# Performance work log

Measured on AMD Instinct MI355X. Metric: run time of the kernel, lower is better.

The kernel has to match this reference:

```python
import jax, jax.numpy as jnp
import numpy as np

N = 50000      # nodes
E = 800000     # edges
DIN = 128
DH = 128
DE = 128
DOUT = 2
EPS = 1e-5     # GraphNorm eps


def _xavier(key, fan_in, fan_out):
    lim = float(np.sqrt(6.0 / (fan_in + fan_out)))
    return jax.random.uniform(key, (fan_in, fan_out), jnp.float32, -lim, lim)


def setup_inputs() -> dict:
    key = jax.random.key(0)
    ks = jax.random.split(key, 8)
    x = jax.random.normal(ks[0], (N, DIN), jnp.float32)
    edge_index = jax.random.randint(ks[1], (2, E), 0, N, dtype=jnp.int32)
    W1 = _xavier(ks[2], DIN, DH); b1 = jnp.zeros((DH,), jnp.float32)
    W2 = _xavier(ks[3], DH, DH);  b2 = jnp.zeros((DH,), jnp.float32)
    W3 = _xavier(ks[4], DH, DE);  b3 = jnp.zeros((DE,), jnp.float32)
    gn1_w = jnp.ones((DH,), jnp.float32); gn1_b = jnp.zeros((DH,), jnp.float32); gn1_a = jnp.ones((DH,), jnp.float32)
    gn2_w = jnp.ones((DH,), jnp.float32); gn2_b = jnp.zeros((DH,), jnp.float32); gn2_a = jnp.ones((DH,), jnp.float32)
    Wout = _xavier(ks[5], DE, DOUT); bout = jnp.zeros((DOUT,), jnp.float32)
    return {
        "x": x, "edge_index": edge_index,
        "W1": W1, "b1": b1, "W2": W2, "b2": b2, "W3": W3, "b3": b3,
        "gn1_w": gn1_w, "gn1_b": gn1_b, "gn1_a": gn1_a,
        "gn2_w": gn2_w, "gn2_b": gn2_b, "gn2_a": gn2_a,
        "Wout": Wout, "bout": bout,
    }


def gcn_conv(x, src, dst, W, b):
    # PyG GCNConv: add self-loops, symmetric normalization, linear, scatter-add at dst.
    n = x.shape[0]
    h = x @ W                                   # [N, C]
    loop = jnp.arange(n, dtype=src.dtype)
    s = jnp.concatenate([src, loop])            # [E+N]
    d = jnp.concatenate([dst, loop])
    deg = jnp.zeros((n,), h.dtype).at[d].add(1.0)
    dinv = jnp.where(deg > 0, jax.lax.rsqrt(deg), 0.0)
    norm = dinv[s] * dinv[d]                    # [E+N]
    out = jnp.zeros_like(h).at[d].add(h[s] * norm[:, None])
    return out + b


def graph_norm(h, w, b, alpha):
    # Single-graph GraphNorm: shift by alpha*mean, normalize by variance of shifted values.
    mean = h.mean(axis=0)
    c = h - alpha * mean
    var = (c * c).mean(axis=0)
    return c * jax.lax.rsqrt(var + EPS) * w + b


def reference(x, edge_index, W1, b1, W2, b2, W3, b3,
              gn1_w, gn1_b, gn1_a, gn2_w, gn2_b, gn2_a, Wout, bout):
    src, dst = edge_index[0], edge_index[1]
    h = gcn_conv(x, src, dst, W1, b1)
    h = jax.nn.relu(graph_norm(h, gn1_w, gn1_b, gn1_a))   # dropout identity (eval)
    h = gcn_conv(h, src, dst, W2, b2)
    h = jax.nn.relu(graph_norm(h, gn2_w, gn2_b, gn2_a))
    h = gcn_conv(h, src, dst, W3, b3)
    return h @ Wout + bout
```

## Files before the change

kernel.cpp:

```cpp
#include <hip/hip_runtime.h>

#define GN_EPS 1e-5f


#define HIST_C 64
#define SCAN_CHUNK 4096
#define LDK 136

typedef __attribute__((ext_vector_type(8))) short short8;
typedef __attribute__((ext_vector_type(4))) float f32x4;

__device__ __forceinline__ unsigned short f2bf(float f) {
    unsigned u = __float_as_uint(f);
    u += 0x7fffu + ((u >> 16) & 1u);
    return (unsigned short)(u >> 16);
}
__device__ __forceinline__ float bflo(unsigned u) { return __uint_as_float(u << 16); }
__device__ __forceinline__ float bfhi(unsigned u) { return __uint_as_float(u & 0xffff0000u); }

__global__ __launch_bounds__(256) void k_prep_hist(const float* __restrict__ W1,
                                                   const float* __restrict__ W2,
                                                   const float* __restrict__ W3,
                                                   const float* __restrict__ Wo,
                                                   const float* __restrict__ b3,
                                                   const float* __restrict__ bo,
                                                   unsigned short* __restrict__ Wt,
                                                   float* __restrict__ M,
                                                   float* __restrict__ mb,
                                                   const int* __restrict__ dst,
                                                   unsigned short* __restrict__ cnt,
                                                   unsigned short* __restrict__ pos,
                                                   int e, int n, int chunk) {
    __shared__ __align__(16) unsigned bins[32768];
    if (blockIdx.x < 2) {
        unsigned short* sT = (unsigned short*)bins;
        const float* W = blockIdx.x == 0 ? W1 : W2;
        unsigned short* o = Wt + blockIdx.x * 16384;
        const float4* W4 = (const float4*)W;
        for (int idx = threadIdx.x; idx < 128 * 32; idx += 256) {
            int k = idx >> 5, c4 = idx & 31;
            float4 v = W4[k * 32 + c4];
            sT[(c4 * 4 + 0) * 130 + k] = f2bf(v.x);
            sT[(c4 * 4 + 1) * 130 + k] = f2bf(v.y);
            sT[(c4 * 4 + 2) * 130 + k] = f2bf(v.z);
            sT[(c4 * 4 + 3) * 130 + k] = f2bf(v.w);
        }
        __syncthreads();
        for (int idx = threadIdx.x; idx < 128 * 128; idx += 256) {
            int c = idx >> 7, k = idx & 127;
            o[idx] = sT[c * 130 + k];
        }
    } else if (blockIdx.x == 2) {
        int k = threadIdx.x;
        if (k < 128) {
            float m0 = 0.f, m1 = 0.f;
            for (int c = 0; c < 128; ++c) {
                float w = W3[k * 128 + c];
                m0 += w * Wo[c * 2];
                m1 += w * Wo[c * 2 + 1];
            }
            M[k * 2] = m0;
            M[k * 2 + 1] = m1;
            if (k < 2) {
                float s = 0.f;
                for (int c = 0; c < 128; ++c) s += b3[c] * Wo[c * 2 + k];
                mb[k] = s + bo[k];
            }
        }
    } else {
        const int c = (int)blockIdx.x - 3;
        const int c0 = c * chunk;
        const int c1 = (c0 + chunk < e) ? c0 + chunk : e;
        const int nw = (n + 1) >> 1;
        for (int i = threadIdx.x; i < nw; i += 256) bins[i] = 0u;
        __syncthreads();
        const bool al = ((size_t)dst & 15) == 0;
        for (int i = c0 + (int)threadIdx.x * 4; i < c1; i += 1024) {
            if (al && i + 3 < c1) {
                int4 d4 = *(const int4*)(dst + i);
                unsigned o0 = atomicAdd(&bins[(unsigned)d4.x >> 1],
                                        (d4.x & 1) ? 0x10000u : 1u);
                unsigned o1 = atomicAdd(&bins[(unsigned)d4.y >> 1],
                                        (d4.y & 1) ? 0x10000u : 1u);
                unsigned o2 = atomicAdd(&bins[(unsigned)d4.z >> 1],
                                        (d4.z & 1) ? 0x10000u : 1u);
                unsigned o3 = atomicAdd(&bins[(unsigned)d4.w >> 1],
                                        (d4.w & 1) ? 0x10000u : 1u);
                ushort4 p;
                p.x = (unsigned short)((o0 >> ((d4.x & 1) * 16)) & 0xffffu);
                p.y = (unsigned short)((o1 >> ((d4.y & 1) * 16)) & 0xffffu);
                p.z = (unsigned short)((o2 >> ((d4.z & 1) * 16)) & 0xffffu);
                p.w = (unsigned short)((o3 >> ((d4.w & 1) * 16)) & 0xffffu);
                *(ushort4*)(pos + i) = p;
            } else {
                for (int k = i; k < c1 && k < i + 4; ++k) {
                    int d = dst[k];
                    unsigned old = atomicAdd(&bins[(unsigned)d >> 1],
                                             (d & 1) ? 0x10000u : 1u);
                    pos[k] = (unsigned short)((old >> ((d & 1) * 16)) & 0xffffu);
                }
            }
        }
        __syncthreads();
        unsigned short* cr = cnt + (size_t)c * n;
        if ((n & 1) == 0) {
            unsigned* cr32 = (unsigned*)cr;
            for (int i = threadIdx.x; i < (n >> 1); i += 256) cr32[i] = bins[i];
        } else {
            for (int i = threadIdx.x; i < n; i += 256)
                cr[i] = (unsigned short)((bins[i >> 1] >> ((i & 1) * 16)) & 0xffffu);
        }
    }
}

__global__ __launch_bounds__(256) void k_reduce(unsigned short* __restrict__ cnt,
                                                int* __restrict__ degi,
                                                int* __restrict__ partial,
                                                int n, int nchunks) {
    int node = blockIdx.x * 256 + threadIdx.x;
    int pdeg = 0;
    if (node < n) {
        int s = 0;
        int cb = 0;
        for (; cb + 8 <= nchunks; cb += 8) {
            int v[8];
            #pragma unroll
            for (int q = 0; q < 8; ++q) v[q] = cnt[(size_t)(cb + q) * n + node];
            #pragma unroll
            for (int q = 0; q < 8; ++q) {
                cnt[(size_t)(cb + q) * n + node] = (unsigned short)s;
                s += v[q];
            }
        }
        for (; cb < nchunks; ++cb) {
            size_t id = (size_t)cb * n + node;
            int v = cnt[id];
            cnt[id] = (unsigned short)s;
            s += v;
        }
        degi[node] = s;
        pdeg = (s + 7) & ~7;
    }
    #pragma unroll
    for (int off = 32; off; off >>= 1) pdeg += __shfl_down(pdeg, off);
    __shared__ int ws[4];
    if ((threadIdx.x & 63) == 0) ws[threadIdx.x >> 6] = pdeg;
    __syncthreads();
    if (threadIdx.x == 0) partial[blockIdx.x] = ws[0] + ws[1] + ws[2] + ws[3];
}

__global__ __launch_bounds__(256) void k_scanfinal(const int* __restrict__ degi,
                                                   const int* __restrict__ partial,
                                                   int* __restrict__ rowptr,
                                                   float* __restrict__ dinv, int n, int nb) {
    int blockbase = 0;
    for (int i = 0; i < (int)blockIdx.x * 16; ++i) blockbase += partial[i];

    int base = blockIdx.x * SCAN_CHUNK + threadIdx.x * 16;
    int v[16], pv[16];
    int s = 0;
    #pragma unroll
    for (int q = 0; q < 16; ++q) {
        int i = base + q;
        v[q] = (i < n) ? degi[i] : 0;
        pv[q] = (v[q] + 7) & ~7;
        s += pv[q];
    }
    const int lane = threadIdx.x & 63;
    const int wid = threadIdx.x >> 6;
    int x = s;
    #pragma unroll
    for (int off = 1; off < 64; off <<= 1) {
        int t = __shfl_up(x, off);
        if (lane >= off) x += t;
    }
    __shared__ int ws[4];
    if (lane == 63) ws[wid] = x;
    __syncthreads();
    int waveoff = 0;
    if (wid > 0) waveoff += ws[0];
    if (wid > 1) waveoff += ws[1];
    if (wid > 2) waveoff += ws[2];
    int excl = x - s + waveoff + blockbase;
    #pragma unroll
    for (int q = 0; q < 16; ++q) {
        int i = base + q;
        if (i < n) {
            rowptr[i] = excl;
            dinv[i] = rsqrtf((float)(v[q] + 1));
        }
        excl += pv[q];
    }
    if ((int)blockIdx.x == nb - 1 && threadIdx.x == 255) {
        rowptr[n] = excl;
    }
}

__global__ void k_fill(const int* __restrict__ src, const int* __restrict__ dst,
                       const unsigned short* __restrict__ pos,
                       const unsigned short* __restrict__ pref,
                       const int* __restrict__ rowptr,
                       const float* __restrict__ dinv,
                       unsigned* __restrict__ csr_ew, int e, int n, int chunk) {
    int base = (blockIdx.x * blockDim.x + threadIdx.x) * 4;
    if (base >= e) return;
    const unsigned short* pr = pref + (size_t)(base / chunk) * n;
    if (base + 3 < e && (((size_t)src & 15) == 0) && (((size_t)dst & 15) == 0)) {
        int4 s4 = *(const int4*)(src + base);
        int4 d4 = *(const int4*)(dst + base);
        ushort4 p4 = *(const ushort4*)(pos + base);
        float as0 = dinv[s4.x], as1 = dinv[s4.y], as2 = dinv[s4.z], as3 = dinv[s4.w];
        float ad0 = dinv[d4.x], ad1 = dinv[d4.y], ad2 = dinv[d4.z], ad3 = dinv[d4.w];
        int b0 = rowptr[d4.x] + pr[d4.x] + p4.x;
        int b1 = rowptr[d4.y] + pr[d4.y] + p4.y;
        int b2 = rowptr[d4.z] + pr[d4.z] + p4.z;
        int b3 = rowptr[d4.w] + pr[d4.w] + p4.w;
        csr_ew[b0] = ((unsigned)s4.x << 16) | (unsigned)f2bf(as0 * ad0);
        csr_ew[b1] = ((unsigned)s4.y << 16) | (unsigned)f2bf(as1 * ad1);
        csr_ew[b2] = ((unsigned)s4.z << 16) | (unsigned)f2bf(as2 * ad2);
        csr_ew[b3] = ((unsigned)s4.w << 16) | (unsigned)f2bf(as3 * ad3);
    } else {
        for (int i = base; i < e && i < base + 4; ++i) {
            int s = src[i], d = dst[i];
            float w = dinv[s] * dinv[d];
            csr_ew[rowptr[d] + (int)pr[d] + (int)pos[i]] =
                ((unsigned)s << 16) | (unsigned)f2bf(w);
        }
    }
}

__global__ __launch_bounds__(256) void k_gemm_f32(const float* __restrict__ X,
                                                  const unsigned short* __restrict__ Wt,
                                                  unsigned short* __restrict__ Y,
                                                  int nrows) {
    __shared__ __align__(16) unsigned short sB[128 * LDK];
    const int t = threadIdx.x;
    const int row0 = blockIdx.x * 64;

    for (int idx = t; idx < 128 * 16; idx += 256) {
        int c = idx >> 4, ch = idx & 15;
        uint4 v = ((const uint4*)(Wt + c * 128))[ch];
        *(uint4*)(&sB[c * LDK + ch * 8]) = v;
    }

    const int w = t >> 6;
    const int lane = t & 63;
    const int m = lane & 15;
    const int quad = lane >> 4;

    const int grow_a = row0 + w * 16 + m;
    const int srow = grow_a < nrows ? grow_a : 0;
    const float4* Xr = (const float4*)(X + (size_t)srow * 128);
    short8 a[4];
    #pragma unroll
    for (int ks = 0; ks < 4; ++ks) {
        int ko4 = ks * 8 + quad * 2;
        float4 v0 = Xr[ko4];
        float4 v1 = Xr[ko4 + 1];
        short8 av;
        av[0] = (short)f2bf(v0.x); av[1] = (short)f2bf(v0.y);
        av[2] = (short)f2bf(v0.z); av[3] = (short)f2bf(v0.w);
        av[4] = (short)f2bf(v1.x); av[5] = (short)f2bf(v1.y);
        av[6] = (short)f2bf(v1.z); av[7] = (short)f2bf(v1.w);
        a[ks] = av;
    }
    __syncthreads();

    f32x4 acc[8] = {};
    #pragma unroll
    for (int ks = 0; ks < 4; ++ks) {
        int ko = ks * 32 + quad * 8;
        #pragma unroll
        for (int ct = 0; ct < 8; ++ct) {
            short8 b = *(const short8*)(&sB[(ct * 16 + m) * LDK + ko]);
            acc[ct] = __builtin_amdgcn_mfma_f32_16x16x32_bf16(a[ks], b, acc[ct], 0, 0, 0);
        }
    }
    #pragma unroll
    for (int r = 0; r < 4; ++r) {
        int grow = row0 + w * 16 + quad * 4 + r;
        if (grow >= nrows) continue;
        unsigned short* yr = Y + (size_t)grow * 128 + m;
        #pragma unroll
        for (int ct = 0; ct < 8; ++ct) yr[ct * 16] = f2bf(acc[ct][r]);
    }
}

__global__ __launch_bounds__(256) void k_gemm_bf(const unsigned short* __restrict__ Xb,
                                                 const unsigned short* __restrict__ Wt,
                                                 unsigned short* __restrict__ Y,
                                                 const float* __restrict__ cs,
                                                 const float* __restrict__ cb,
                                                 int nrows) {
    __shared__ __align__(16) unsigned short sB[128 * LDK];
    const int t = threadIdx.x;
    const int row0 = blockIdx.x * 64;

    for (int idx = t; idx < 128 * 16; idx += 256) {
        int c = idx >> 4, ch = idx & 15;
        uint4 v = ((const uint4*)(Wt + c * 128))[ch];
        *(uint4*)(&sB[c * LDK + ch * 8]) = v;
    }

    const int w = t >> 6;
    const int lane = t & 63;
    const int m = lane & 15;
    const int quad = lane >> 4;

    const int grow_a = row0 + w * 16 + m;
    const int srow = grow_a < nrows ? grow_a : 0;
    const uint4* Xr = (const uint4*)(Xb + (size_t)srow * 128);
    short8 a[4];
    #pragma unroll
    for (int ks = 0; ks < 4; ++ks) {
        uint4 u = Xr[ks * 4 + quad];
        int kf = (ks * 32 + quad * 8) >> 2;
        float4 s0 = ((const float4*)cs)[kf];
        float4 s1 = ((const float4*)cs)[kf + 1];
        float4 c0 = ((const float4*)cb)[kf];
        float4 c1 = ((const float4*)cb)[kf + 1];
        short8 av;
        av[0] = (short)f2bf(fmaxf(fmaf(bflo(u.x), s0.x, c0.x), 0.f));
        av[1] = (short)f2bf(fmaxf(fmaf(bfhi(u.x), s0.y, c0.y), 0.f));
        av[2] = (short)f2bf(fmaxf(fmaf(bflo(u.y), s0.z, c0.z), 0.f));
        av[3] = (short)f2bf(fmaxf(fmaf(bfhi(u.y), s0.w, c0.w), 0.f));
        av[4] = (short)f2bf(fmaxf(fmaf(bflo(u.z), s1.x, c1.x), 0.f));
        av[5] = (short)f2bf(fmaxf(fmaf(bfhi(u.z), s1.y, c1.y), 0.f));
        av[6] = (short)f2bf(fmaxf(fmaf(bflo(u.w), s1.z, c1.z), 0.f));
        av[7] = (short)f2bf(fmaxf(fmaf(bfhi(u.w), s1.w, c1.w), 0.f));
        a[ks] = av;
    }
    __syncthreads();

    f32x4 acc[8] = {};
    #pragma unroll
    for (int ks = 0; ks < 4; ++ks) {
        int ko = ks * 32 + quad * 8;
        #pragma unroll
        for (int ct = 0; ct < 8; ++ct) {
            short8 b = *(const short8*)(&sB[(ct * 16 + m) * LDK + ko]);
            acc[ct] = __builtin_amdgcn_mfma_f32_16x16x32_bf16(a[ks], b, acc[ct], 0, 0, 0);
        }
    }
    #pragma unroll
    for (int r = 0; r < 4; ++r) {
        int grow = row0 + w * 16 + quad * 4 + r;
        if (grow >= nrows) continue;
        unsigned short* yr = Y + (size_t)grow * 128 + m;
        #pragma unroll
        for (int ct = 0; ct < 8; ++ct) yr[ct * 16] = f2bf(acc[ct][r]);
    }
}

__global__ __launch_bounds__(256) void k_gather(const unsigned short* __restrict__ H,
                                                unsigned short* __restrict__ O,
                                                const int* __restrict__ rowptr,
                                                const unsigned* __restrict__ csr_ew,
                                                const float* __restrict__ dinv,
                                                const float* __restrict__ bias,
                                                float* __restrict__ pS,
                                                float* __restrict__ pQ, int n) {
    __shared__ float sS[4][128];
    __shared__ float sQ[4][128];
    const int wid = threadIdx.x >> 6;
    const int node = blockIdx.x * 4 + wid;
    const int lane = threadIdx.x & 63;
    const int qw = lane >> 4;
    const int ql = lane & 15;
    const uint4* Hx = (const uint4*)H;
    float acc[8] = {};
    if (node < n) {
        float di = dinv[node];
        if (qw == 0) {
            uint4 u = Hx[(size_t)node * 16 + ql];
            float dd = di * di;
            float4 ba = ((const float4*)bias)[ql * 2];
            float4 bb = ((const float4*)bias)[ql * 2 + 1];
            acc[0] = bflo(u.x) * dd + ba.x; acc[1] = bfhi(u.x) * dd + ba.y;
            acc[2] = bflo(u.y) * dd + ba.z; acc[3] = bfhi(u.y) * dd + ba.w;
            acc[4] = bflo(u.z) * dd + bb.x; acc[5] = bfhi(u.z) * dd + bb.y;
            acc[6] = bflo(u.w) * dd + bb.z; acc[7] = bfhi(u.w) * dd + bb.w;
        }
        int j = rowptr[node];
        const int end = rowptr[node + 1];
        for (; j + 16 <= end; j += 16) {
            unsigned ew[4];
            #pragma unroll
            for (int q = 0; q < 4; ++q) ew[q] = csr_ew[j + 4 * q + qw];
            uint4 u[4];
            #pragma unroll
            for (int q = 0; q < 4; ++q)
                u[q] = Hx[((ew[q] >> 12) & 0xFFFF0u) + (unsigned)ql];
            #pragma unroll
            for (int q = 0; q < 4; ++q) {
                float nr = __uint_as_float(ew[q] << 16);
                acc[0] += bflo(u[q].x) * nr; acc[1] += bfhi(u[q].x) * nr;
                acc[2] += bflo(u[q].y) * nr; acc[3] += bfhi(u[q].y) * nr;
                acc[4] += bflo(u[q].z) * nr; acc[5] += bfhi(u[q].z) * nr;
                acc[6] += bflo(u[q].w) * nr; acc[7] += bfhi(u[q].w) * nr;
            }
        }
        if (j < end) {
            unsigned ew[2];
            #pragma unroll
            for (int q = 0; q < 2; ++q) ew[q] = csr_ew[j + qw * 2 + q];
            uint4 u[2];
            #pragma unroll
            for (int q = 0; q < 2; ++q)
                u[q] = Hx[((ew[q] >> 12) & 0xFFFF0u) + (unsigned)ql];
            #pragma unroll
            for (int q = 0; q < 2; ++q) {
                float nr = __uint_as_float(ew[q] << 16);
                acc[0] += bflo(u[q].x) * nr; acc[1] += bfhi(u[q].x) * nr;
                acc[2] += bflo(u[q].y) * nr; acc[3] += bfhi(u[q].y) * nr;
                acc[4] += bflo(u[q].z) * nr; acc[5] += bfhi(u[q].z) * nr;
                acc[6] += bflo(u[q].w) * nr; acc[7] += bfhi(u[q].w) * nr;
            }
        }
        #pragma unroll
        for (int i = 0; i < 8; ++i) {
            acc[i] += __shfl_down(acc[i], 32);
            acc[i] += __shfl_down(acc[i], 16);
        }
    }
    if (qw == 0) {
        if (node < n) {
            unsigned short h[8];
            float v[8];
            #pragma unroll
            for (int i = 0; i < 8; ++i) {
                h[i] = f2bf(acc[i]);
                v[i] = __uint_as_float((unsigned)h[i] << 16);
                sS[wid][ql * 8 + i] = v[i];
                sQ[wid][ql * 8 + i] = v[i] * v[i];
            }
            uint4 o;
            o.x = (unsigned)h[0] | ((unsigned)h[1] << 16);
            o.y = (unsigned)h[2] | ((unsigned)h[3] << 16);
            o.z = (unsigned)h[4] | ((unsigned)h[5] << 16);
            o.w = (unsigned)h[6] | ((unsigned)h[7] << 16);
            *(uint4*)(O + (size_t)node * 128 + ql * 8) = o;
        } else {
            #pragma unroll
            for (int i = 0; i < 8; ++i) {
                sS[wid][ql * 8 + i] = 0.f;
                sQ[wid][ql * 8 + i] = 0.f;
            }
        }
    }
    __syncthreads();
    const int t = threadIdx.x;
    if (t < 128) {
        float s = sS[0][t] + sS[1][t] + sS[2][t] + sS[3][t];
        float q = sQ[0][t] + sQ[1][t] + sQ[2][t] + sQ[3][t];
        const int slotb = (blockIdx.x & 63) << 7;
        atomicAdd(&pS[slotb + t], s);
        atomicAdd(&pQ[slotb + t], q);
    }
}

__global__ __launch_bounds__(256) void k_zproj(const unsigned short* __restrict__ Xb,
                                               const float* __restrict__ M,
                                               const float* __restrict__ cs,
                                               const float* __restrict__ cb,
                                               float2* __restrict__ Z, int n) {
    int node = blockIdx.x * 4 + (threadIdx.x >> 6);
    if (node >= n) return;
    int lane = threadIdx.x & 63;
    unsigned u = ((const unsigned*)Xb)[(size_t)node * 64 + lane];
    int c0 = lane * 2;
    float a = fmaxf(fmaf(bflo(u), cs[c0], cb[c0]), 0.f);
    float b = fmaxf(fmaf(bfhi(u), cs[c0 + 1], cb[c0 + 1]), 0.f);
    float p0 = a * M[c0 * 2]     + b * M[(c0 + 1) * 2];
    float p1 = a * M[c0 * 2 + 1] + b * M[(c0 + 1) * 2 + 1];
    #pragma unroll
    for (int off = 32; off; off >>= 1) {
        p0 += __shfl_down(p0, off);
        p1 += __shfl_down(p1, off);
    }
    if (lane == 0) Z[node] = make_float2(p0, p1);
}

__global__ __launch_bounds__(256) void k_gatherZ(const float2* __restrict__ Z,
                                                 const int* __restrict__ rowptr,
                                                 const unsigned* __restrict__ csr_ew,
                                                 const float* __restrict__ dinv,
                                                 const float* __restrict__ mb,
                                                 float* __restrict__ out, int n) {
    int wid = threadIdx.x >> 6;
    int lane = threadIdx.x & 63;
    int g = lane >> 4;
    int gl = lane & 15;
    int node = blockIdx.x * 16 + wid * 4 + g;
    if (node >= n) return;
    float2 acc = make_float2(0.f, 0.f);
    if (gl == 0) {
        float di = dinv[node];
        float2 z = Z[node];
        acc.x = z.x * di * di + mb[0];
        acc.y = z.y * di * di + mb[1];
    }
    int j = rowptr[node];
    const int end = rowptr[node + 1];
    for (int jj = j + gl; jj < end; jj += 16) {
        unsigned ew = csr_ew[jj];
        float2 z = Z[ew >> 16];
        float w = __uint_as_float(ew << 16);
        acc.x += z.x * w;
        acc.y += z.y * w;
    }
    #pragma unroll
    for (int off = 8; off; off >>= 1) {
        acc.x += __shfl_down(acc.x, off);
        acc.y += __shfl_down(acc.y, off);
    }
    if (gl == 0) {
        out[(size_t)node * 2]     = acc.x;
        out[(size_t)node * 2 + 1] = acc.y;
    }
}

__global__ void k_finstats(const float* __restrict__ pS, const float* __restrict__ pQ,
                           const float* __restrict__ w, const float* __restrict__ b,
                           const float* __restrict__ alpha,
                           float* __restrict__ colscale, float* __restrict__ colshift,
                           int n) {
    int c = threadIdx.x;
    if (c >= 128) return;
    float s = 0.f, q = 0.f;
    #pragma unroll 8
    for (int blk = 0; blk < 64; ++blk) {
        s += pS[blk * 128 + c];
        q += pQ[blk * 128 + c];
    }
    float inv_n = 1.0f / (float)n;
    float m = s * inv_n;
    float eh2 = q * inv_n;
    float a = alpha[c];
    float var = eh2 - (2.0f * a - a * a) * m * m;
    float scale = rsqrtf(var + GN_EPS) * w[c];
    colscale[c] = scale;
    colshift[c] = b[c] - a * m * scale;
}

extern "C" void kernel_launch(void* const* d_in, const int* in_sizes, int n_in,
                              void* d_out, int out_size, void* d_ws, size_t ws_size,
                              hipStream_t stream) {
    const float* x    = (const float*)d_in[0];
    const int*   ei   = (const int*)  d_in[1];
    const float* W1   = (const float*)d_in[2];
    const float* b1   = (const float*)d_in[3];
    const float* W2   = (const float*)d_in[4];
    const float* b2   = (const float*)d_in[5];
    const float* W3   = (const float*)d_in[6];
    const float* b3   = (const float*)d_in[7];
    const float* gn1w = (const float*)d_in[8];
    const float* gn1b = (const float*)d_in[9];
    const float* gn1a = (const float*)d_in[10];
    const float* gn2w = (const float*)d_in[11];
    const float* gn2b = (const float*)d_in[12];
    const float* gn2a = (const float*)d_in[13];
    const float* Wout = (const float*)d_in[14];
    const float* bout = (const float*)d_in[15];
    float* out = (float*)d_out;

    const int n = in_sizes[0] / 128;
    const int e = in_sizes[1] / 2;
    const int* srcI = ei;
    const int* dstI = ei + e;

    const int chunk = (((e + HIST_C - 1) / HIST_C) + 3) & ~3;
    const int nchunks = (e + chunk - 1) / chunk;

    char* base = (char*)d_ws;
    size_t off = 0;
    auto take = [&](size_t bytes) -> void* {
        void* r = base + off;
        off += (bytes + 15) & ~(size_t)15;
        return r;
    };
    unsigned short* bufH = (unsigned short*)take((size_t)n * 256);
    unsigned short* bufG = (unsigned short*)take((size_t)n * 256);
    float* dinv     = (float*)take((size_t)n * 4);
    float* colscale = (float*)take(128 * 4);
    float* colshift = (float*)take(128 * 4);
    int*   rowptr   = (int*)take(((size_t)n + 1) * 4);
    int*   partial  = (int*)take(256 * 4);
    unsigned short* Wt = (unsigned short*)take(2 * 16384 * 2);
    float* M        = (float*)take(256 * 4);
    float* mb       = (float*)take(2 * 4);
    float2* Z       = (float2*)take((size_t)n * 8);
    int*   degi     = (int*)take((size_t)n * 4);
    unsigned short* cnt = (unsigned short*)take((size_t)nchunks * n * 2);
    unsigned short* pos = (unsigned short*)take((size_t)e * 2);
    float* pS       = (float*)take(2 * 64 * 128 * 4);
    float* pQ       = (float*)take(2 * 64 * 128 * 4);
    size_t csr_cap  = (size_t)e + 8 * (size_t)n;
    unsigned* csr_ew = (unsigned*)take(csr_cap * 4);
    size_t zbytes   = (size_t)((base + off) - (char*)pS);

    const int nb = (n + SCAN_CHUNK - 1) / SCAN_CHUNK;
    const int gemmGrid = (n + 63) / 64;
    const int gathGrid = (n + 3) / 4;

    hipMemsetAsync(pS, 0, zbytes, stream);
    k_prep_hist<<<3 + nchunks, 256, 0, stream>>>(W1, W2, W3, Wout, b3, bout,
                                                 Wt, M, mb, dstI, cnt, pos, e, n, chunk);
    k_reduce<<<(n + 255) / 256, 256, 0, stream>>>(cnt, degi, partial, n, nchunks);
    k_scanfinal<<<nb, 256, 0, stream>>>(degi, partial, rowptr, dinv, n, nb);
    k_fill<<<(e + 1023) / 1024, 256, 0, stream>>>(srcI, dstI, pos, cnt, rowptr,
                                                  dinv, csr_ew, e, n, chunk);

    k_gemm_f32<<<gemmGrid, 256, 0, stream>>>(x, Wt, bufH, n);
    k_gather<<<gathGrid, 256, 0, stream>>>(bufH, bufG, rowptr, csr_ew, dinv, b1, pS, pQ, n);
    k_finstats<<<1, 128, 0, stream>>>(pS, pQ, gn1w, gn1b, gn1a, colscale, colshift, n);

    k_gemm_bf<<<gemmGrid, 256, 0, stream>>>(bufG, Wt + 16384, bufH, colscale, colshift, n);
    k_gather<<<gathGrid, 256, 0, stream>>>(bufH, bufG, rowptr, csr_ew, dinv, b2,
                                           pS + 8192, pQ + 8192, n);
    k_finstats<<<1, 128, 0, stream>>>(pS + 8192, pQ + 8192, gn2w, gn2b, gn2a,
                                      colscale, colshift, n);

    k_zproj<<<gathGrid, 256, 0, stream>>>(bufG, M, colscale, colshift, Z, n);
    k_gatherZ<<<(n + 15) / 16, 256, 0, stream>>>(Z, rowptr, csr_ew, dinv, mb, out, n);
}
```

Baseline: 265.9 us.

## Fuse CSR fill with first GEMM, inline GraphNorm stats, drop memset

```diff
diff --git a/kernel.cpp b/kernel.cpp
--- a/kernel.cpp
+++ b/kernel.cpp
@@ -27,6 +27,8 @@
                                                    unsigned short* __restrict__ Wt,
                                                    float* __restrict__ M,
                                                    float* __restrict__ mb,
+                                                   float* __restrict__ pS,
+                                                   float* __restrict__ pQ,
                                                    const int* __restrict__ dst,
                                                    unsigned short* __restrict__ cnt,
                                                    unsigned short* __restrict__ pos,
@@ -51,6 +53,11 @@
             o[idx] = sT[c * 130 + k];
         }
     } else if (blockIdx.x == 2) {
+        float4 z4 = make_float4(0.f, 0.f, 0.f, 0.f);
+        for (int i = threadIdx.x; i < 4096; i += 256) {
+            ((float4*)pS)[i] = z4;
+            ((float4*)pQ)[i] = z4;
+        }
         int k = threadIdx.x;
         if (k < 128) {
             float m0 = 0.f, m1 = 0.f;
@@ -152,7 +159,9 @@
 __global__ __launch_bounds__(256) void k_scanfinal(const int* __restrict__ degi,
                                                    const int* __restrict__ partial,
                                                    int* __restrict__ rowptr,
-                                                   float* __restrict__ dinv, int n, int nb) {
+                                                   float* __restrict__ dinv,
+                                                   unsigned* __restrict__ csr_ew,
+                                                   int n, int nb) {
     int blockbase = 0;
     for (int i = 0; i < (int)blockIdx.x * 16; ++i) blockbase += partial[i];
 
@@ -188,6 +197,7 @@
         if (i < n) {
             rowptr[i] = excl;
             dinv[i] = rsqrtf((float)(v[q] + 1));
+            for (int z = v[q]; z < pv[q]; ++z) csr_ew[excl + z] = 0u;
         }
         excl += pv[q];
     }
@@ -196,46 +206,63 @@
     }
 }
 
-__global__ void k_fill(const int* __restrict__ src, const int* __restrict__ dst,
-                       const unsigned short* __restrict__ pos,
-                       const unsigned short* __restrict__ pref,
-                       const int* __restrict__ rowptr,
-                       const float* __restrict__ dinv,
-                       unsigned* __restrict__ csr_ew, int e, int n, int chunk) {
-    int base = (blockIdx.x * blockDim.x + threadIdx.x) * 4;
-    if (base >= e) return;
-    const unsigned short* pr = pref + (size_t)(base / chunk) * n;
-    if (base + 3 < e && (((size_t)src & 15) == 0) && (((size_t)dst & 15) == 0)) {
-        int4 s4 = *(const int4*)(src + base);
-        int4 d4 = *(const int4*)(dst + base);
-        ushort4 p4 = *(const ushort4*)(pos + base);
-        float as0 = dinv[s4.x], as1 = dinv[s4.y], as2 = dinv[s4.z], as3 = dinv[s4.w];
-        float ad0 = dinv[d4.x], ad1 = dinv[d4.y], ad2 = dinv[d4.z], ad3 = dinv[d4.w];
-        int b0 = rowptr[d4.x] + pr[d4.x] + p4.x;
-        int b1 = rowptr[d4.y] + pr[d4.y] + p4.y;
-        int b2 = rowptr[d4.z] + pr[d4.z] + p4.z;
-        int b3 = rowptr[d4.w] + pr[d4.w] + p4.w;
-        csr_ew[b0] = ((unsigned)s4.x << 16) | (unsigned)f2bf(as0 * ad0);
-        csr_ew[b1] = ((unsigned)s4.y << 16) | (unsigned)f2bf(as1 * ad1);
-        csr_ew[b2] = ((unsigned)s4.z << 16) | (unsigned)f2bf(as2 * ad2);
-        csr_ew[b3] = ((unsigned)s4.w << 16) | (unsigned)f2bf(as3 * ad3);
-    } else {
-        for (int i = base; i < e && i < base + 4; ++i) {
-            int s = src[i], d = dst[i];
-            float w = dinv[s] * dinv[d];
-            csr_ew[rowptr[d] + (int)pr[d] + (int)pos[i]] =
-                ((unsigned)s << 16) | (unsigned)f2bf(w);
-        }
-    }
-}
-
-__global__ __launch_bounds__(256) void k_gemm_f32(const float* __restrict__ X,
+__global__ __launch_bounds__(256) void k_fillgemm(const float* __restrict__ X,
                                                   const unsigned short* __restrict__ Wt,
                                                   unsigned short* __restrict__ Y,
-                                                  int nrows) {
+                                                  const int* __restrict__ src,
+                                                  const int* __restrict__ dst,
+                                                  const unsigned short* __restrict__ pos,
+                                                  const unsigned short* __restrict__ pref,
+                                                  const int* __restrict__ rowptr,
+                                                  const float* __restrict__ dinv,
+                                                  unsigned* __restrict__ csr_ew,
+                                                  int nrows, int e, int chunk, int n,
+                                                  int ngemm, int nfill) {
     __shared__ __align__(16) unsigned short sB[128 * LDK];
+
+    int mn2 = (ngemm < nfill ? ngemm : nfill) * 2;
+    bool isg;
+    int bid;
+    if ((int)blockIdx.x < mn2) {
+        isg = (blockIdx.x & 1) == 0;
+        bid = blockIdx.x >> 1;
+    } else {
+        int r = (int)blockIdx.x - mn2;
+        isg = ngemm > nfill;
+        bid = (mn2 >> 1) + r;
+    }
+
+    if (!isg) {
+        int base = (bid * 256 + (int)threadIdx.x) * 4;
+        if (base >= e) return;
+        const unsigned short* pr = pref + (size_t)(base / chunk) * n;
+        if (base + 3 < e && (((size_t)src & 15) == 0) && (((size_t)dst & 15) == 0)) {
+            int4 s4 = *(const int4*)(src + base);
+            int4 d4 = *(const int4*)(dst + base);
+            ushort4 p4 = *(const ushort4*)(pos + base);
+            float as0 = dinv[s4.x], as1 = dinv[s4.y], as2 = dinv[s4.z], as3 = dinv[s4.w];
+            float ad0 = dinv[d4.x], ad1 = dinv[d4.y], ad2 = dinv[d4.z], ad3 = dinv[d4.w];
+            int b0 = rowptr[d4.x] + pr[d4.x] + p4.x;
+            int b1 = rowptr[d4.y] + pr[d4.y] + p4.y;
+            int b2 = rowptr[d4.z] + pr[d4.z] + p4.z;
+            int b3 = rowptr[d4.w] + pr[d4.w] + p4.w;
+            csr_ew[b0] = ((unsigned)s4.x << 16) | (unsigned)f2bf(as0 * ad0);
+            csr_ew[b1] = ((unsigned)s4.y << 16) | (unsigned)f2bf(as1 * ad1);
+            csr_ew[b2] = ((unsigned)s4.z << 16) | (unsigned)f2bf(as2 * ad2);
+            csr_ew[b3] = ((unsigned)s4.w << 16) | (unsigned)f2bf(as3 * ad3);
+        } else {
+            for (int i = base; i < e && i < base + 4; ++i) {
+                int s = src[i], d = dst[i];
+                float w = dinv[s] * dinv[d];
+                csr_ew[rowptr[d] + (int)pr[d] + (int)pos[i]] =
+                    ((unsigned)s << 16) | (unsigned)f2bf(w);
+            }
+        }
+        return;
+    }
+
     const int t = threadIdx.x;
-    const int row0 = blockIdx.x * 64;
+    const int row0 = bid * 64;
 
     for (int idx = t; idx < 128 * 16; idx += 256) {
         int c = idx >> 4, ch = idx & 15;
@@ -286,21 +313,54 @@
     }
 }
 
+__device__ __forceinline__ void finstats_lds(const float* __restrict__ pS,
+                                             const float* __restrict__ pQ,
+                                             const float* __restrict__ gw,
+                                             const float* __restrict__ gb,
+                                             const float* __restrict__ ga,
+                                             float* __restrict__ sCS,
+                                             float* __restrict__ sCB, int n) {
+    int c = threadIdx.x;
+    if (c < 128) {
+        float s = 0.f, q = 0.f;
+        #pragma unroll 8
+        for (int blk = 0; blk < 64; ++blk) {
+            s += pS[blk * 128 + c];
+            q += pQ[blk * 128 + c];
+        }
+        float inv_n = 1.0f / (float)n;
+        float m = s * inv_n;
+        float eh2 = q * inv_n;
+        float a = ga[c];
+        float var = eh2 - (2.0f * a - a * a) * m * m;
+        float scale = rsqrtf(var + GN_EPS) * gw[c];
+        sCS[c] = scale;
+        sCB[c] = gb[c] - a * m * scale;
+    }
+}
+
 __global__ __launch_bounds__(256) void k_gemm_bf(const unsigned short* __restrict__ Xb,
                                                  const unsigned short* __restrict__ Wt,
                                                  unsigned short* __restrict__ Y,
-                                                 const float* __restrict__ cs,
-                                                 const float* __restrict__ cb,
-                                                 int nrows) {
+                                                 const float* __restrict__ pS,
+                                                 const float* __restrict__ pQ,
+                                                 const float* __restrict__ gw,
+                                                 const float* __restrict__ gb,
+                                                 const float* __restrict__ ga,
+                                                 int nrows, int n) {
     __shared__ __align__(16) unsigned short sB[128 * LDK];
+    __shared__ __align__(16) float sCS[128];
+    __shared__ __align__(16) float sCB[128];
     const int t = threadIdx.x;
     const int row0 = blockIdx.x * 64;
 
+    finstats_lds(pS, pQ, gw, gb, ga, sCS, sCB, n);
     for (int idx = t; idx < 128 * 16; idx += 256) {
         int c = idx >> 4, ch = idx & 15;
         uint4 v = ((const uint4*)(Wt + c * 128))[ch];
         *(uint4*)(&sB[c * LDK + ch * 8]) = v;
     }
+    __syncthreads();
 
     const int w = t >> 6;
     const int lane = t & 63;
@@ -315,10 +375,10 @@
     for (int ks = 0; ks < 4; ++ks) {
         uint4 u = Xr[ks * 4 + quad];
         int kf = (ks * 32 + quad * 8) >> 2;
-        float4 s0 = ((const float4*)cs)[kf];
-        float4 s1 = ((const float4*)cs)[kf + 1];
-        float4 c0 = ((const float4*)cb)[kf];
-        float4 c1 = ((const float4*)cb)[kf + 1];
+        float4 s0 = ((const float4*)sCS)[kf];
+        float4 s1 = ((const float4*)sCS)[kf + 1];
+        float4 c0 = ((const float4*)sCB)[kf];
+        float4 c1 = ((const float4*)sCB)[kf + 1];
         short8 av;
         av[0] = (short)f2bf(fmaxf(fmaf(bflo(u.x), s0.x, c0.x), 0.f));
         av[1] = (short)f2bf(fmaxf(fmaf(bfhi(u.x), s0.y, c0.y), 0.f));
@@ -330,7 +390,6 @@
         av[7] = (short)f2bf(fmaxf(fmaf(bfhi(u.w), s1.w, c1.w), 0.f));
         a[ks] = av;
     }
-    __syncthreads();
 
     f32x4 acc[8] = {};
     #pragma unroll
@@ -461,24 +520,46 @@
 
 __global__ __launch_bounds__(256) void k_zproj(const unsigned short* __restrict__ Xb,
                                                const float* __restrict__ M,
-                                               const float* __restrict__ cs,
-                                               const float* __restrict__ cb,
+                                               const float* __restrict__ pS,
+                                               const float* __restrict__ pQ,
+                                               const float* __restrict__ gw,
+                                               const float* __restrict__ gb,
+                                               const float* __restrict__ ga,
                                                float2* __restrict__ Z, int n) {
-    int node = blockIdx.x * 4 + (threadIdx.x >> 6);
-    if (node >= n) return;
-    int lane = threadIdx.x & 63;
-    unsigned u = ((const unsigned*)Xb)[(size_t)node * 64 + lane];
-    int c0 = lane * 2;
-    float a = fmaxf(fmaf(bflo(u), cs[c0], cb[c0]), 0.f);
-    float b = fmaxf(fmaf(bfhi(u), cs[c0 + 1], cb[c0 + 1]), 0.f);
-    float p0 = a * M[c0 * 2]     + b * M[(c0 + 1) * 2];
-    float p1 = a * M[c0 * 2 + 1] + b * M[(c0 + 1) * 2 + 1];
-    #pragma unroll
-    for (int off = 32; off; off >>= 1) {
-        p0 += __shfl_down(p0, off);
-        p1 += __shfl_down(p1, off);
-    }
-    if (lane == 0) Z[node] = make_float2(p0, p1);
+    __shared__ __align__(16) float sCS[128];
+    __shared__ __align__(16) float sCB[128];
+    __shared__ __align__(16) float sM[256];
+    finstats_lds(pS, pQ, gw, gb, ga, sCS, sCB, n);
+    if (threadIdx.x < 128) {
+        sM[threadIdx.x * 2] = M[threadIdx.x * 2];
+        sM[threadIdx.x * 2 + 1] = M[threadIdx.x * 2 + 1];
+    }
+    __syncthreads();
+
+    const int wid = threadIdx.x >> 6;
+    const int lane = threadIdx.x & 63;
+    const int c0 = lane * 2;
+    const float cs0 = sCS[c0], cs1 = sCS[c0 + 1];
+    const float cb0 = sCB[c0], cb1 = sCB[c0 + 1];
+    const float m00 = sM[c0 * 2], m01 = sM[c0 * 2 + 1];
+    const float m10 = sM[(c0 + 1) * 2], m11 = sM[(c0 + 1) * 2 + 1];
+
+    #pragma unroll
+    for (int p = 0; p < 16; ++p) {
+        int node = (int)blockIdx.x * 64 + p * 4 + wid;
+        if (node >= n) break;
+        unsigned u = ((const unsigned*)Xb)[(size_t)node * 64 + lane];
+        float a = fmaxf(fmaf(bflo(u), cs0, cb0), 0.f);
+        float b = fmaxf(fmaf(bfhi(u), cs1, cb1), 0.f);
+        float p0 = a * m00 + b * m10;
+        float p1 = a * m01 + b * m11;
+        #pragma unroll
+        for (int off = 32; off; off >>= 1) {
+            p0 += __shfl_down(p0, off);
+            p1 += __shfl_down(p1, off);
+        }
+        if (lane == 0) Z[node] = make_float2(p0, p1);
+    }
 }
 
 __global__ __launch_bounds__(256) void k_gatherZ(const float2* __restrict__ Z,
@@ -518,29 +599,6 @@
         out[(size_t)node * 2]     = acc.x;
         out[(size_t)node * 2 + 1] = acc.y;
     }
-}
-
-__global__ void k_finstats(const float* __restrict__ pS, const float* __restrict__ pQ,
-                           const float* __restrict__ w, const float* __restrict__ b,
-                           const float* __restrict__ alpha,
-                           float* __restrict__ colscale, float* __restrict__ colshift,
-                           int n) {
-    int c = threadIdx.x;
-    if (c >= 128) return;
-    float s = 0.f, q = 0.f;
-    #pragma unroll 8
-    for (int blk = 0; blk < 64; ++blk) {
-        s += pS[blk * 128 + c];
-        q += pQ[blk * 128 + c];
-    }
-    float inv_n = 1.0f / (float)n;
-    float m = s * inv_n;
-    float eh2 = q * inv_n;
-    float a = alpha[c];
-    float var = eh2 - (2.0f * a - a * a) * m * m;
-    float scale = rsqrtf(var + GN_EPS) * w[c];
-    colscale[c] = scale;
-    colshift[c] = b[c] - a * m * scale;
 }
 
 extern "C" void kernel_launch(void* const* d_in, const int* in_sizes, int n_in,
@@ -582,8 +640,6 @@
     unsigned short* bufH = (unsigned short*)take((size_t)n * 256);
     unsigned short* bufG = (unsigned short*)take((size_t)n * 256);
     float* dinv     = (float*)take((size_t)n * 4);
-    float* colscale = (float*)take(128 * 4);
-    float* colshift = (float*)take(128 * 4);
     int*   rowptr   = (int*)take(((size_t)n + 1) * 4);
     int*   partial  = (int*)take(256 * 4);
     unsigned short* Wt = (unsigned short*)take(2 * 16384 * 2);
@@ -597,30 +653,29 @@
     float* pQ       = (float*)take(2 * 64 * 128 * 4);
     size_t csr_cap  = (size_t)e + 8 * (size_t)n;
     unsigned* csr_ew = (unsigned*)take(csr_cap * 4);
-    size_t zbytes   = (size_t)((base + off) - (char*)pS);
 
     const int nb = (n + SCAN_CHUNK - 1) / SCAN_CHUNK;
     const int gemmGrid = (n + 63) / 64;
+    const int fillGrid = (e + 1023) / 1024;
     const int gathGrid = (n + 3) / 4;
 
-    hipMemsetAsync(pS, 0, zbytes, stream);
     k_prep_hist<<<3 + nchunks, 256, 0, stream>>>(W1, W2, W3, Wout, b3, bout,
-                                                 Wt, M, mb, dstI, cnt, pos, e, n, chunk);
+                                                 Wt, M, mb, pS, pQ, dstI, cnt, pos,
+                                                 e, n, chunk);
     k_reduce<<<(n + 255) / 256, 256, 0, stream>>>(cnt, degi, partial, n, nchunks);
-    k_scanfinal<<<nb, 256, 0, stream>>>(degi, partial, rowptr, dinv, n, nb);
-    k_fill<<<(e + 1023) / 1024, 256, 0, stream>>>(srcI, dstI, pos, cnt, rowptr,
-                                                  dinv, csr_ew, e, n, chunk);
-
-    k_gemm_f32<<<gemmGrid, 256, 0, stream>>>(x, Wt, bufH, n);
+    k_scanfinal<<<nb, 256, 0, stream>>>(degi, partial, rowptr, dinv, csr_ew, n, nb);
+
+    k_fillgemm<<<gemmGrid + fillGrid, 256, 0, stream>>>(x, Wt, bufH, srcI, dstI,
+                                                        pos, cnt, rowptr, dinv, csr_ew,
+                                                        n, e, chunk, n, gemmGrid, fillGrid);
     k_gather<<<gathGrid, 256, 0, stream>>>(bufH, bufG, rowptr, csr_ew, dinv, b1, pS, pQ, n);
-    k_finstats<<<1, 128, 0, stream>>>(pS, pQ, gn1w, gn1b, gn1a, colscale, colshift, n);
-
-    k_gemm_bf<<<gemmGrid, 256, 0, stream>>>(bufG, Wt + 16384, bufH, colscale, colshift, n);
+
+    k_gemm_bf<<<gemmGrid, 256, 0, stream>>>(bufG, Wt + 16384, bufH, pS, pQ,
+                                            gn1w, gn1b, gn1a, n, n);
     k_gather<<<gathGrid, 256, 0, stream>>>(bufH, bufG, rowptr, csr_ew, dinv, b2,
                                            pS + 8192, pQ + 8192, n);
-    k_finstats<<<1, 128, 0, stream>>>(pS + 8192, pQ + 8192, gn2w, gn2b, gn2a,
-                                      colscale, colshift, n);
-
-    k_zproj<<<gathGrid, 256, 0, stream>>>(bufG, M, colscale, colshift, Z, n);
+
+    k_zproj<<<(n + 63) / 64, 256, 0, stream>>>(bufG, M, pS + 8192, pQ + 8192,
+                                               gn2w, gn2b, gn2a, Z, n);
     k_gatherZ<<<(n + 15) / 16, 256, 0, stream>>>(Z, rowptr, csr_ew, dinv, mb, out, n);
 }
```

Result: no change. 270.6 us (+1.7%).
